# Optimization experiments

Hardware: AMD Instinct MI355X
Metric: run time of the kernel (lower is better)

## Reference

```python
import jax, jax.numpy as jnp
import numpy as np

ALPHA = 0.2          # LeakyReLU negative slope
NEG_INF = -9e15      # mask fill value used by the original module

def setup_inputs() -> dict:
    key = jax.random.key(0)
    k1, k2, k3, k4 = jax.random.split(key, 4)
    B, N, F_in, F_out = 8, 2048, 64, 64
    inp = jax.random.normal(k1, (B, N, F_in), dtype=jnp.float32)
    adj = jax.random.randint(k2, (B, N, N), 0, 2, dtype=jnp.int32)
    # Parameters (kaiming-normal-ish init)
    W = jax.random.normal(k3, (F_in, F_out), dtype=jnp.float32) * np.sqrt(2.0 / F_in)
    a = jax.random.normal(k4, (2 * F_out, 1), dtype=jnp.float32) * np.sqrt(2.0 / (2 * F_out))
    return {"inp": inp, "adj": adj, "W": W, "a": a}

def reference(inp, adj, W, a):
    # h: [B, N, F_out]
    h = jnp.matmul(inp, W)
    F_out = W.shape[1]
    a1 = a[:F_out, 0]   # [F_out]
    a2 = a[F_out:, 0]   # [F_out]
    # e[b,i,j] = leakyrelu(h[b,i]·a1 + h[b,j]·a2)  -- broadcasted, avoids O(N^2*2F) concat
    f1 = h @ a1         # [B, N]
    f2 = h @ a2         # [B, N]
    e = jax.nn.leaky_relu(f1[:, :, None] + f2[:, None, :], negative_slope=ALPHA)
    scores = jnp.where(adj > 0, e, NEG_INF)
    attention = jax.nn.softmax(scores, axis=-1)  # [B, N, N]
    # dropout omitted (deterministic eval-mode reference)
    h_prime = jnp.matmul(attention, h)           # [B, N, F_out]
    return jax.nn.elu(h_prime)                   # concat=True path
```

## Files before the change

kernel.cpp:

```cpp
#include <hip/hip_runtime.h>
#include <hip/hip_bf16.h>

#define ALPHA 0.2f

constexpr int B = 8, N = 2048, F = 64;

typedef __attribute__((ext_vector_type(8))) short bf16x8;
typedef __attribute__((ext_vector_type(16))) float f32x16;

__device__ __forceinline__ float lrelu(float x) { return fmaxf(x, ALPHA * x); }

__global__ __launch_bounds__(256) void k1_project(
    const float* __restrict__ inp, const float* __restrict__ W,
    const float* __restrict__ a,
    __hip_bfloat16* __restrict__ hT, float* __restrict__ f1, float* __restrict__ f2)
{
  __shared__ float Wl[64][64];
  __shared__ float inpl[32][64];
  __shared__ float red[32][8][2];
  __shared__ __hip_bfloat16 hl[32][64];
  __shared__ float al[128];

  const int tid = threadIdx.x;
  const int g0 = blockIdx.x * 32;
  const int b = g0 / N, i0 = g0 % N;

  #pragma unroll
  for (int m = 0; m < 4; ++m) {
    int off = m * 1024 + tid * 4;
    *(float4*)((float*)Wl + off) = *(const float4*)(W + off);
  }
  #pragma unroll
  for (int m = 0; m < 2; ++m) {
    int off = m * 1024 + tid * 4;
    *(float4*)((float*)inpl + off) = *(const float4*)(inp + (size_t)g0 * F + off);
  }
  if (tid < 128) al[tid] = a[tid];
  __syncthreads();

  const int r = tid >> 3, c0 = (tid & 7) * 8;
  float acc[8];
  #pragma unroll
  for (int c = 0; c < 8; ++c) acc[c] = 0.f;
  for (int k = 0; k < 64; ++k) {
    float v = inpl[r][k];
    #pragma unroll
    for (int c = 0; c < 8; ++c) acc[c] += v * Wl[k][c0 + c];
  }
  float p1 = 0.f, p2 = 0.f;
  unsigned short hb[8] __attribute__((aligned(16)));
  #pragma unroll
  for (int c = 0; c < 8; ++c) {
    p1 += acc[c] * al[c0 + c];
    p2 += acc[c] * al[64 + c0 + c];
    __hip_bfloat16 hv = __float2bfloat16(acc[c]);
    hb[c] = *(unsigned short*)&hv;
  }
  red[r][tid & 7][0] = p1;
  red[r][tid & 7][1] = p2;
  *(uint4*)&hl[r][c0] = *(uint4*)hb;
  __syncthreads();

  if (tid < 32) {
    float s1 = 0.f, s2 = 0.f;
    #pragma unroll
    for (int m = 0; m < 8; ++m) { s1 += red[tid][m][0]; s2 += red[tid][m][1]; }
    f1[g0 + tid] = s1;
    f2[g0 + tid] = s2;
  }
  const int c = tid >> 2, r8 = (tid & 3) * 8;
  unsigned short tb[8] __attribute__((aligned(16)));
  #pragma unroll
  for (int m = 0; m < 8; ++m) tb[m] = *(unsigned short*)&hl[r8 + m][c];
  const int jb = i0 + r8;
  const int jsw = (jb & ~127) | ((jb & 127) ^ ((c & 7) << 3));
  *(uint4*)(hT + ((size_t)b * F + c) * N + jsw) = *(uint4*)tb;
}

__global__ __launch_bounds__(256) void k2_f2max(const float* __restrict__ f2,
                                                float* __restrict__ f2max)
{
  __shared__ float s[256];
  const int b = blockIdx.x, tid = threadIdx.x;
  float m = -1e30f;
  for (int j = tid; j < N; j += 256) m = fmaxf(m, f2[b * N + j]);
  s[tid] = m;
  __syncthreads();
  for (int w = 128; w > 0; w >>= 1) {
    if (tid < w) s[tid] = fmaxf(s[tid], s[tid + w]);
    __syncthreads();
  }
  if (tid == 0) f2max[b] = s[0];
}

__global__ __launch_bounds__(256) void k3_attn(
    const int* __restrict__ adj, const __hip_bfloat16* __restrict__ hT,
    const float* __restrict__ f1, const float* __restrict__ f2,
    const float* __restrict__ f2max, float* __restrict__ out)
{
  constexpr int RT = 32, JT = 128, NT = N / JT;
  __shared__ __hip_bfloat16 Pl[2][RT][JT];
  __shared__ __hip_bfloat16 Hl[2][F][JT];
  __shared__ float rs[RT][8];
  __shared__ float rcp_s[RT];
  __shared__ float redt[2][32][32];

  const int tid = threadIdx.x;
  const int lane = tid & 63, wid = tid >> 6;
  const int ct = wid >> 1, kh = wid & 1;
  const int bi = blockIdx.x;
  const int b = bi / (N / RT);
  const int i0 = (bi % (N / RT)) * RT;

  const int r = tid >> 3, jc = (tid & 7) * 16;
  const float f1r = f1[b * N + i0 + r];
  const float Mr = lrelu(f1r + f2max[b]);

  const int* adjrow = adj + ((size_t)(b * N + i0 + r)) * N + jc;
  const float* f2row = f2 + b * N + jc;
  const int swp = (r & 7) << 3;

  const __hip_bfloat16* hsrc =
      hT + ((size_t)b * F + (wid * 16 + (lane >> 4))) * N + (lane & 15) * 8;

  float rowsum = 0.f;
  f32x16 acc;
  #pragma unroll
  for (int q = 0; q < 16; ++q) acc[q] = 0.f;

  #define STAGE_H(T, BUFI)                                                      \
    do {                                                                        \
      const __hip_bfloat16* s0_ = hsrc + (T) * JT;                              \
      char* lb_ = (char*)(&Hl[(BUFI)][0][0]) + wid * 4096;                      \
      _Pragma("unroll")                                                         \
      for (int q_ = 0; q_ < 4; ++q_) {                                          \
        __builtin_amdgcn_global_load_lds(                                       \
            (const __attribute__((address_space(1))) void*)(s0_ + q_ * 4 * N),  \
            (__attribute__((address_space(3))) void*)(lb_ + q_ * 1024),         \
            16, 0, 0);                                                          \
      }                                                                         \
    } while (0)

  int4 av[4]; float4 fv[4];
  #pragma unroll
  for (int m = 0; m < 4; ++m) {
    av[m] = *(const int4*)(adjrow + m * 4);
    fv[m] = *(const float4*)(f2row + m * 4);
  }
  STAGE_H(0, 0);

  for (int t = 0; t < NT; ++t) {
    const int buf = t & 1;
    const bool more = (t + 1 < NT);
    int4 avn[4]; float4 fvn[4];
    if (more) {
      #pragma unroll
      for (int m = 0; m < 4; ++m) {
        avn[m] = *(const int4*)(adjrow + (t + 1) * JT + m * 4);
        fvn[m] = *(const float4*)(f2row + (t + 1) * JT + m * 4);
      }
    }

    unsigned short pb[16] __attribute__((aligned(16)));
    #pragma unroll
    for (int m = 0; m < 4; ++m) {
      const int* ai = (const int*)&av[m];
      const float* fe = (const float*)&fv[m];
      #pragma unroll
      for (int e = 0; e < 4; ++e) {
        float s = lrelu(f1r + fe[e]);
        float p = (ai[e] > 0) ? __expf(s - Mr) : 0.f;
        __hip_bfloat16 pbf = __float2bfloat16(p);
        rowsum += __bfloat162float(pbf);
        pb[m * 4 + e] = *(unsigned short*)&pbf;
      }
    }
    *(uint4*)&Pl[buf][r][jc ^ swp]       = *(uint4*)&pb[0];
    *(uint4*)&Pl[buf][r][(jc + 8) ^ swp] = *(uint4*)&pb[8];

    __syncthreads();

    if (more) STAGE_H(t + 1, buf ^ 1);

    const int arow = lane & 31;
    const int bcol = ct * 32 + (lane & 31);
    const int klo = kh * 64 + ((lane >> 5) * 8);
    #pragma unroll
    for (int s = 0; s < 4; ++s) {
      const int ak = klo + s * 16;
      bf16x8 af  = *(const bf16x8*)&Pl[buf][arow][ak ^ ((arow & 7) << 3)];
      bf16x8 bfr = *(const bf16x8*)&Hl[buf][bcol][ak ^ ((bcol & 7) << 3)];
      asm volatile("v_mfma_f32_32x32x16_bf16 %0, %1, %2, %0"
                   : "+v"(acc) : "v"(af), "v"(bfr));
    }

    if (more) {
      #pragma unroll
      for (int m = 0; m < 4; ++m) { av[m] = avn[m]; fv[m] = fvn[m]; }
    }
  }
  #undef STAGE_H

  rs[r][tid & 7] = rowsum;
  if (kh == 1) {
    #pragma unroll
    for (int q = 0; q < 16; ++q)
      redt[ct][(q & 3) + 8 * (q >> 2) + 4 * (lane >> 5)][lane & 31] = acc[q];
  }
  __syncthreads();
  if (tid < 32) {
    float s = 0.f;
    #pragma unroll
    for (int m = 0; m < 8; ++m) s += rs[tid][m];
    rcp_s[tid] = 1.0f / fmaxf(s, 1e-30f);
  }
  __syncthreads();
  if (kh == 0) {
    #pragma unroll
    for (int q = 0; q < 16; ++q) {
      const int row = (q & 3) + 8 * (q >> 2) + 4 * (lane >> 5);
      float v = (acc[q] + redt[ct][row][lane & 31]) * rcp_s[row];
      v = v > 0.f ? v : expm1f(v);
      out[((size_t)(b * N + i0 + row)) * F + ct * 32 + (lane & 31)] = v;
    }
  }
}

extern "C" void kernel_launch(void* const* d_in, const int* in_sizes, int n_in,
                              void* d_out, int out_size, void* d_ws, size_t ws_size,
                              hipStream_t stream) {
  const float* inp = (const float*)d_in[0];
  const int*   adj = (const int*)d_in[1];
  const float* W   = (const float*)d_in[2];
  const float* a   = (const float*)d_in[3];
  float* out = (float*)d_out;

  char* ws = (char*)d_ws;
  __hip_bfloat16* hT = (__hip_bfloat16*)ws;
  float* f1  = (float*)(ws + (size_t)B * F * N * sizeof(__hip_bfloat16));
  float* f2  = f1 + (size_t)B * N;
  float* f2m = f2 + (size_t)B * N;

  hipLaunchKernelGGL(k1_project, dim3(B * N / 32), dim3(256), 0, stream, inp, W, a, hT, f1, f2);
  hipLaunchKernelGGL(k2_f2max, dim3(B), dim3(256), 0, stream, f2, f2m);
  hipLaunchKernelGGL(k3_attn, dim3(B * N / 32), dim3(256), 0, stream, adj, hT, f1, f2, f2m, out);
}
```

Baseline: 60.31 us.

## Coalesce adjacency loads and prefetch two tiles ahead in attention kernel

Changes the per-thread column mapping so that the 8 threads of a row read adjacent 16-byte chunks (stride 32 elements between chunks), which improves coalescing of the int32 adjacency and f2 loads. The main loop is also unrolled by two with fixed register sets, so loads for tile t+2 are issued right after the barrier, giving a deeper prefetch. The costs are more live registers, which may lower occupancy, and narrower 8-byte LDS stores for the P tile.

```diff
diff --git a/kernel.cpp b/kernel.cpp
--- a/kernel.cpp
+++ b/kernel.cpp
@@ -112,12 +112,12 @@
   const int b = bi / (N / RT);
   const int i0 = (bi % (N / RT)) * RT;
 
-  const int r = tid >> 3, jc = (tid & 7) * 16;
+  const int r = tid >> 3, q = tid & 7;
   const float f1r = f1[b * N + i0 + r];
   const float Mr = lrelu(f1r + f2max[b]);
 
-  const int* adjrow = adj + ((size_t)(b * N + i0 + r)) * N + jc;
-  const float* f2row = f2 + b * N + jc;
+  const int* adjrow = adj + ((size_t)(b * N + i0 + r)) * N + 4 * q;
+  const float* f2base = f2 + b * N + 4 * q;
   const int swp = (r & 7) << 3;
 
   const __hip_bfloat16* hsrc =
@@ -126,7 +126,11 @@
   float rowsum = 0.f;
   f32x16 acc;
   #pragma unroll
-  for (int q = 0; q < 16; ++q) acc[q] = 0.f;
+  for (int z = 0; z < 16; ++z) acc[z] = 0.f;
+
+  const int arow = lane & 31;
+  const int bcol = ct * 32 + (lane & 31);
+  const int klo = kh * 64 + ((lane >> 5) * 8);
 
   #define STAGE_H(T, BUFI)                                                      \
     do {                                                                        \
@@ -141,71 +145,63 @@
       }                                                                         \
     } while (0)
 
-  int4 av[4]; float4 fv[4];
-  #pragma unroll
-  for (int m = 0; m < 4; ++m) {
-    av[m] = *(const int4*)(adjrow + m * 4);
-    fv[m] = *(const float4*)(f2row + m * 4);
-  }
+  #define LOADSET(AV, FV, T)                                                    \
+    do {                                                                        \
+      _Pragma("unroll")                                                         \
+      for (int m_ = 0; m_ < 4; ++m_) {                                          \
+        AV[m_] = *(const int4*)(adjrow + (T) * JT + 32 * m_);                   \
+        FV[m_] = *(const float4*)(f2base + (T) * JT + 32 * m_);                 \
+      }                                                                         \
+    } while (0)
+
+  #define ITER(T, AV, FV, BUF)                                                  \
+    do {                                                                        \
+      _Pragma("unroll")                                                         \
+      for (int m_ = 0; m_ < 4; ++m_) {                                          \
+        const int* ai_ = (const int*)&AV[m_];                                   \
+        const float* fe_ = (const float*)&FV[m_];                               \
+        unsigned short pbm_[4] __attribute__((aligned(8)));                     \
+        _Pragma("unroll")                                                       \
+        for (int e_ = 0; e_ < 4; ++e_) {                                        \
+          float s_ = lrelu(f1r + fe_[e_]);                                      \
+          float p_ = (ai_[e_] > 0) ? __expf(s_ - Mr) : 0.f;                     \
+          __hip_bfloat16 pbf_ = __float2bfloat16(p_);                           \
+          rowsum += __bfloat162float(pbf_);                                     \
+          pbm_[e_] = *(unsigned short*)&pbf_;                                   \
+        }                                                                       \
+        *(uint2*)&Pl[BUF][r][(4 * q + 32 * m_) ^ swp] = *(uint2*)pbm_;          \
+      }                                                                         \
+      __syncthreads();                                                          \
+      if ((T) + 1 < NT) STAGE_H((T) + 1, (BUF) ^ 1);                            \
+      if ((T) + 2 < NT) LOADSET(AV, FV, (T) + 2);                               \
+      _Pragma("unroll")                                                         \
+      for (int s_ = 0; s_ < 4; ++s_) {                                          \
+        const int ak_ = klo + s_ * 16;                                          \
+        bf16x8 af_ = *(const bf16x8*)&Pl[BUF][arow][ak_ ^ ((arow & 7) << 3)];   \
+        bf16x8 bf_ = *(const bf16x8*)&Hl[BUF][bcol][ak_ ^ ((bcol & 7) << 3)];   \
+        asm volatile("v_mfma_f32_32x32x16_bf16 %0, %1, %2, %0"                  \
+                     : "+v"(acc) : "v"(af_), "v"(bf_));                         \
+      }                                                                         \
+    } while (0)
+
+  int4 a0v[4], a1v[4]; float4 g0v[4], g1v[4];
+  LOADSET(a0v, g0v, 0);
+  LOADSET(a1v, g1v, 1);
   STAGE_H(0, 0);
 
-  for (int t = 0; t < NT; ++t) {
-    const int buf = t & 1;
-    const bool more = (t + 1 < NT);
-    int4 avn[4]; float4 fvn[4];
-    if (more) {
-      #pragma unroll
-      for (int m = 0; m < 4; ++m) {
-        avn[m] = *(const int4*)(adjrow + (t + 1) * JT + m * 4);
-        fvn[m] = *(const float4*)(f2row + (t + 1) * JT + m * 4);
-      }
-    }
-
-    unsigned short pb[16] __attribute__((aligned(16)));
-    #pragma unroll
-    for (int m = 0; m < 4; ++m) {
-      const int* ai = (const int*)&av[m];
-      const float* fe = (const float*)&fv[m];
-      #pragma unroll
-      for (int e = 0; e < 4; ++e) {
-        float s = lrelu(f1r + fe[e]);
-        float p = (ai[e] > 0) ? __expf(s - Mr) : 0.f;
-        __hip_bfloat16 pbf = __float2bfloat16(p);
-        rowsum += __bfloat162float(pbf);
-        pb[m * 4 + e] = *(unsigned short*)&pbf;
-      }
-    }
-    *(uint4*)&Pl[buf][r][jc ^ swp]       = *(uint4*)&pb[0];
-    *(uint4*)&Pl[buf][r][(jc + 8) ^ swp] = *(uint4*)&pb[8];
-
-    __syncthreads();
-
-    if (more) STAGE_H(t + 1, buf ^ 1);
-
-    const int arow = lane & 31;
-    const int bcol = ct * 32 + (lane & 31);
-    const int klo = kh * 64 + ((lane >> 5) * 8);
-    #pragma unroll
-    for (int s = 0; s < 4; ++s) {
-      const int ak = klo + s * 16;
-      bf16x8 af  = *(const bf16x8*)&Pl[buf][arow][ak ^ ((arow & 7) << 3)];
-      bf16x8 bfr = *(const bf16x8*)&Hl[buf][bcol][ak ^ ((bcol & 7) << 3)];
-      asm volatile("v_mfma_f32_32x32x16_bf16 %0, %1, %2, %0"
-                   : "+v"(acc) : "v"(af), "v"(bfr));
-    }
-
-    if (more) {
-      #pragma unroll
-      for (int m = 0; m < 4; ++m) { av[m] = avn[m]; fv[m] = fvn[m]; }
-    }
-  }
+  for (int t = 0; t < NT; t += 2) {
+    ITER(t,     a0v, g0v, 0);
+    ITER(t + 1, a1v, g1v, 1);
+  }
+  #undef ITER
+  #undef LOADSET
   #undef STAGE_H
 
-  rs[r][tid & 7] = rowsum;
+  rs[r][q] = rowsum;
   if (kh == 1) {
     #pragma unroll
-    for (int q = 0; q < 16; ++q)
-      redt[ct][(q & 3) + 8 * (q >> 2) + 4 * (lane >> 5)][lane & 31] = acc[q];
+    for (int z = 0; z < 16; ++z)
+      redt[ct][(z & 3) + 8 * (z >> 2) + 4 * (lane >> 5)][lane & 31] = acc[z];
   }
   __syncthreads();
   if (tid < 32) {
@@ -217,9 +213,9 @@
   __syncthreads();
   if (kh == 0) {
     #pragma unroll
-    for (int q = 0; q < 16; ++q) {
-      const int row = (q & 3) + 8 * (q >> 2) + 4 * (lane >> 5);
-      float v = (acc[q] + redt[ct][row][lane & 31]) * rcp_s[row];
+    for (int z = 0; z < 16; ++z) {
+      const int row = (z & 3) + 8 * (z >> 2) + 4 * (lane >> 5);
+      float v = (acc[z] + redt[ct][row][lane & 31]) * rcp_s[row];
       v = v > 0.f ? v : expm1f(v);
       out[((size_t)(b * N + i0 + row)) * F + ct * 32 + (lane & 31)] = v;
     }
```

Result: no change. 59.32 us (-1.6%).
